# Kernel optimization log

Measured on AMD Instinct MI355X. Metric: run time of the kernel, lower is better.

The kernel has to match this reference:

```python
import jax, jax.numpy as jnp
import numpy as np

HEAD_DIM = 128
HIDDEN = 5120
NUM_KV_GROUPS = 8
NUM_MODALITIES = 3
NUM_Q_HEADS = 40
QKV_PER_MOD = NUM_Q_HEADS * HEAD_DIM + 2 * NUM_KV_GROUPS * HEAD_DIM + NUM_Q_HEADS  # 7208


def _rms_norm(x, w, eps=1e-6):
    xf = x.astype(jnp.float32)
    inv = jax.lax.rsqrt(jnp.mean(xf * xf, axis=-1, keepdims=True) + eps)
    return (xf * inv).astype(x.dtype) * w


def _apply_rope(x, cos, sin):
    # x: [B,S,H,D], cos/sin: [B,S,rd]
    rd = cos.shape[-1]
    xr, xp = x[..., :rd], x[..., rd:]
    c, s = cos[:, :, None, :], sin[:, :, None, :]
    x1, x2 = xr[..., : rd // 2], xr[..., rd // 2:]
    rot = jnp.concatenate([-x2, x1], axis=-1)
    return jnp.concatenate([xr * c + rot * s, xp], axis=-1)


def setup_inputs() -> dict:
    key = jax.random.key(0)
    ks = jax.random.split(key, 6)
    B, S = 1, 2048
    return {
        "x": jax.random.normal(ks[0], (B, S, HIDDEN), jnp.float32),
        "rope_cos": jax.random.uniform(ks[1], (B, S, HEAD_DIM), jnp.float32),
        "rope_sin": jax.random.uniform(ks[2], (B, S, HEAD_DIM), jnp.float32),
        "modality_ids": jax.random.randint(ks[3], (B, S), 0, NUM_MODALITIES, jnp.int32),
        "pre_norm": jnp.ones((NUM_MODALITIES * HIDDEN,), jnp.float32),
        "qkv_w": jax.random.normal(ks[4], (NUM_MODALITIES * QKV_PER_MOD, HIDDEN), jnp.float32) * 0.02,
        "q_norm": jnp.ones((NUM_MODALITIES * HEAD_DIM,), jnp.float32),
        "k_norm": jnp.ones((NUM_MODALITIES * HEAD_DIM,), jnp.float32),
        "proj_w": jax.random.normal(ks[5], (NUM_MODALITIES * HIDDEN, HIDDEN), jnp.float32) * 0.02,
    }


def reference(x, rope_cos, rope_sin, modality_ids, pre_norm, qkv_w, q_norm, k_norm, proj_w):
    B, S, _ = x.shape
    # per-token modality gather of pre-norm weight
    norm_w = pre_norm.reshape(NUM_MODALITIES, HIDDEN)[modality_ids]  # [B,S,H]
    normed = _rms_norm(x, norm_w)

    # modality-routed QKV: compute all modalities, select with one-hot (dense, jit-friendly)
    oh = jax.nn.one_hot(modality_ids, NUM_MODALITIES, dtype=x.dtype)  # [B,S,M]
    qkv_w3 = qkv_w.reshape(NUM_MODALITIES, QKV_PER_MOD, HIDDEN)
    qkv_all = jnp.einsum("bsh,moh->bsmo", normed, qkv_w3)  # [B,S,M,QKV]
    qkv = jnp.einsum("bsm,bsmo->bso", oh, qkv_all)

    q_dim = NUM_Q_HEADS * HEAD_DIM
    k_dim = NUM_KV_GROUPS * HEAD_DIM
    q = qkv[..., :q_dim].reshape(B, S, NUM_Q_HEADS, HEAD_DIM)
    k = qkv[..., q_dim:q_dim + k_dim].reshape(B, S, NUM_KV_GROUPS, HEAD_DIM)
    v = qkv[..., q_dim + k_dim:q_dim + 2 * k_dim].reshape(B, S, NUM_KV_GROUPS, HEAD_DIM)
    gate = jax.nn.sigmoid(qkv[..., q_dim + 2 * k_dim:q_dim + 2 * k_dim + NUM_Q_HEADS])  # [B,S,NQ]

    qn = q_norm.reshape(NUM_MODALITIES, HEAD_DIM)[modality_ids][:, :, None, :]  # [B,S,1,D]
    kn = k_norm.reshape(NUM_MODALITIES, HEAD_DIM)[modality_ids][:, :, None, :]
    q = _rms_norm(q, qn)
    k = _rms_norm(k, kn)

    q = _apply_rope(q, rope_cos, rope_sin)
    k = _apply_rope(k, rope_cos, rope_sin)

    repeat = NUM_Q_HEADS // NUM_KV_GROUPS
    k = jnp.repeat(k, repeat, axis=2)  # [B,S,NQ,D]
    v = jnp.repeat(v, repeat, axis=2)

    scale = 1.0 / np.sqrt(HEAD_DIM)
    scores = jnp.einsum("bqhd,bkhd->bhqk", q, k) * scale  # [B,NQ,S,S]
    attn = jax.nn.softmax(scores, axis=-1)
    out = jnp.einsum("bhqk,bkhd->bqhd", attn, v)  # [B,S,NQ,D]

    out = (out * gate[..., None]).reshape(B, S, NUM_Q_HEADS * HEAD_DIM)

    proj_w3 = proj_w.reshape(NUM_MODALITIES, HIDDEN, HIDDEN)
    proj_all = jnp.einsum("bsh,moh->bsmo", out, proj_w3)  # [B,S,M,H]
    return jnp.einsum("bsm,bsmo->bso", oh, proj_all)
```

## Files before the change

### kernel.cpp

```cpp
#include <hip/hip_runtime.h>

typedef _Float16 f16;
typedef f16 f16x8 __attribute__((ext_vector_type(8)));
typedef f16 f16x4 __attribute__((ext_vector_type(4)));
typedef float f32x4 __attribute__((ext_vector_type(4)));

#define HID 5120
#define QKVO 7208
#define S_TOK 2048
#define NQH 40
#define NKV 8
#define HD 128

__device__ __forceinline__ void gload16(const void* g, void* l) {
    __builtin_amdgcn_global_load_lds(
        (const __attribute__((address_space(1))) void*)g,
        (__attribute__((address_space(3))) void*)l,
        16, 0, 0);
}

__global__ void sort_tokens(const int* __restrict__ mod, int* __restrict__ sorted,
                            int* __restrict__ offs)
{
    int tid = threadIdx.x, wave = tid >> 6, lane = tid & 63;
    int mloc[8];
    int c[3] = {0, 0, 0};
#pragma unroll
    for (int j = 0; j < 8; ++j) {
        int m = mod[tid * 8 + j];
        mloc[j] = m;
        c[m]++;
    }
    __shared__ int wsum[4][3];
    int excl[3];
#pragma unroll
    for (int m = 0; m < 3; ++m) {
        int v = c[m];
        int incl = v;
        for (int d = 1; d < 64; d <<= 1) {
            int n = __shfl_up(incl, d, 64);
            if (lane >= d) incl += n;
        }
        excl[m] = incl - v;
        if (lane == 63) wsum[wave][m] = incl;
    }
    __syncthreads();
    int wbase[3], tot[3];
#pragma unroll
    for (int m = 0; m < 3; ++m) {
        int b = 0, t = 0;
        for (int w = 0; w < 4; ++w) {
            if (w < wave) b += wsum[w][m];
            t += wsum[w][m];
        }
        wbase[m] = b;
        tot[m] = t;
    }
    int base[3];
    base[0] = 0;
    base[1] = tot[0];
    base[2] = tot[0] + tot[1];
    if (tid == 0) {
        offs[0] = 0;
        offs[1] = tot[0];
        offs[2] = tot[0] + tot[1];
        offs[3] = S_TOK;
    }
    int pos[3];
#pragma unroll
    for (int m = 0; m < 3; ++m) pos[m] = base[m] + wbase[m] + excl[m];
#pragma unroll
    for (int j = 0; j < 8; ++j) {
        int m = mloc[j];
        sorted[pos[m]++] = tid * 8 + j;
    }
}

__global__ void cvt_f32_f16(const float* __restrict__ src, f16* __restrict__ dst, int n4)
{
    int i = blockIdx.x * 256 + threadIdx.x;
    int stride = gridDim.x * 256;
    const float4* s4 = (const float4*)src;
    f16x4* d4 = (f16x4*)dst;
    for (; i < n4; i += stride) {
        float4 a = s4[i];
        f16x4 h;
        h[0] = (f16)a.x; h[1] = (f16)a.y; h[2] = (f16)a.z; h[3] = (f16)a.w;
        d4[i] = h;
    }
}

__global__ void rms_pre(const float* __restrict__ x, const int* __restrict__ mod,
                        const float* __restrict__ prenorm, f16* __restrict__ A1)
{
    int tok = blockIdx.x, tid = threadIdx.x;
    int m = mod[tok];
    const float4* xv = (const float4*)(x + (size_t)tok * HID);
    float4 v[5];
    float ss = 0.f;
#pragma unroll
    for (int j = 0; j < 5; ++j) {
        v[j] = xv[tid + 256 * j];
        ss += v[j].x * v[j].x + v[j].y * v[j].y + v[j].z * v[j].z + v[j].w * v[j].w;
    }
    for (int d = 1; d < 64; d <<= 1) ss += __shfl_xor(ss, d, 64);
    __shared__ float ws[4];
    if ((tid & 63) == 0) ws[tid >> 6] = ss;
    __syncthreads();
    float tot = ws[0] + ws[1] + ws[2] + ws[3];
    float inv = rsqrtf(tot * (1.f / HID) + 1e-6f);
    const float4* wv = (const float4*)(prenorm + (size_t)m * HID);
    f16x4* out4 = (f16x4*)(A1 + (size_t)tok * HID);
#pragma unroll
    for (int j = 0; j < 5; ++j) {
        float4 w = wv[tid + 256 * j];
        f16x4 h;
        h[0] = (f16)(v[j].x * inv * w.x);
        h[1] = (f16)(v[j].y * inv * w.y);
        h[2] = (f16)(v[j].z * inv * w.z);
        h[3] = (f16)(v[j].w * inv * w.w);
        out4[tid + 256 * j] = h;
    }
}

__global__ void gemm_grouped(const f16* __restrict__ A, const f16* __restrict__ W,
                             float* __restrict__ C,
                             const int* __restrict__ sorted_tok,
                             const int* __restrict__ mod_off, int NW, int NTN, int NPAN)
{
    const int K = HID;
    int F = blockIdx.x;
    int g = F & 7, s = F >> 3;
    int P = (s >> 4) * 8 + g;
    if (P >= NPAN) return;
    int mt = s & 15;
    int nt = P % NTN, mod = P / NTN;
    int off = mod_off[mod], cnt = mod_off[mod + 1] - off;
    if (mt * 128 >= cnt) return;
    __shared__ __align__(16) f16 As[128 * 64];
    __shared__ __align__(16) f16 Bs[128 * 64];
    __shared__ int rowtok[128];
    int tid = threadIdx.x, wave = tid >> 6, lane = tid & 63;
    if (tid < 128) {
        int r = mt * 128 + tid;
        rowtok[tid] = (r < cnt) ? sorted_tok[off + r] : -1;
    }
    __syncthreads();
    int wr = wave >> 1, wc = wave & 1;
    f32x4 acc[4][4] = {};
    const f16* Wm = W + (size_t)mod * NW * K;
    for (int kt = 0; kt < K / 64; ++kt) {
        int k0 = kt * 64;
#pragma unroll
        for (int it = 0; it < 4; ++it) {
            int c = it * 256 + tid;
            int row = c >> 3, kc = c & 7, skc = kc ^ (row & 7);
            int tk = rowtok[row];
            if (tk < 0) tk = 0;
            gload16(A + (size_t)tk * K + k0 + skc * 8, &As[c * 8]);
        }
#pragma unroll
        for (int it = 0; it < 4; ++it) {
            int c = it * 256 + tid;
            int row = c >> 3, kc = c & 7, skc = kc ^ (row & 7);
            int o = nt * 128 + row;
            if (o >= NW) o = NW - 1;
            gload16(Wm + (size_t)o * K + k0 + skc * 8, &Bs[c * 8]);
        }
        __syncthreads();
#pragma unroll
        for (int ks = 0; ks < 2; ++ks) {
            f16x8 a[4], b[4];
#pragma unroll
            for (int i = 0; i < 4; ++i) {
                int ar = wr * 64 + i * 16 + (lane & 15);
                int ac = (ks * 4 + (lane >> 4)) ^ (ar & 7);
                a[i] = *(const f16x8*)&As[ar * 64 + ac * 8];
                int br = wc * 64 + i * 16 + (lane & 15);
                int bc = (ks * 4 + (lane >> 4)) ^ (br & 7);
                b[i] = *(const f16x8*)&Bs[br * 64 + bc * 8];
            }
#pragma unroll
            for (int mi = 0; mi < 4; ++mi)
#pragma unroll
                for (int nj = 0; nj < 4; ++nj)
                    acc[mi][nj] = __builtin_amdgcn_mfma_f32_16x16x32_f16(
                        a[mi], b[nj], acc[mi][nj], 0, 0, 0);
        }
        __syncthreads();
    }
    int cl = lane & 15, rg = lane >> 4;
#pragma unroll
    for (int mi = 0; mi < 4; ++mi) {
#pragma unroll
        for (int rr = 0; rr < 4; ++rr) {
            int row = wr * 64 + mi * 16 + rg * 4 + rr;
            int tk = rowtok[row];
            if (tk < 0) continue;
            float* crow = C + (size_t)tk * NW;
#pragma unroll
            for (int nj = 0; nj < 4; ++nj) {
                int o = nt * 128 + wc * 64 + nj * 16 + cl;
                if (o < NW) crow[o] = acc[mi][nj][rr];
            }
        }
    }
}

__global__ void qkv_post(const float* __restrict__ qkv, const int* __restrict__ mod,
                         const float* __restrict__ cosb, const float* __restrict__ sinb,
                         const float* __restrict__ qnorm, const float* __restrict__ knorm,
                         f16* __restrict__ Qb, f16* __restrict__ Kb, float* __restrict__ gateb)
{
    int tok = blockIdx.x, tid = threadIdx.x;
    int wave = tid >> 6, lane = tid & 63;
    int m = mod[tok];
    float c0 = cosb[tok * HD + lane], c1 = cosb[tok * HD + 64 + lane];
    float s0 = sinb[tok * HD + lane], s1 = sinb[tok * HD + 64 + lane];
    const float* row = qkv + (size_t)tok * QKVO;
    for (int u = wave; u < 48; u += 4) {
        int base = (u < 40) ? u * HD : NQH * HD + (u - 40) * HD;
        float x0 = row[base + lane];
        float x1 = row[base + 64 + lane];
        float ss = x0 * x0 + x1 * x1;
        for (int d = 1; d < 64; d <<= 1) ss += __shfl_xor(ss, d, 64);
        float inv = rsqrtf(ss * (1.f / HD) + 1e-6f);
        const float* nw = (u < 40 ? qnorm : knorm) + m * HD;
        float n0 = x0 * inv * nw[lane];
        float n1 = x1 * inv * nw[64 + lane];
        float r0 = n0 * c0 - n1 * s0;
        float r1 = n1 * c1 + n0 * s1;
        if (u < 40) {
            const float sc = 0.08838834764831845f;
            r0 *= sc; r1 *= sc;
            Qb[((size_t)u * S_TOK + tok) * HD + lane] = (f16)r0;
            Qb[((size_t)u * S_TOK + tok) * HD + 64 + lane] = (f16)r1;
        } else {
            Kb[((size_t)(u - 40) * S_TOK + tok) * HD + lane] = (f16)r0;
            Kb[((size_t)(u - 40) * S_TOK + tok) * HD + 64 + lane] = (f16)r1;
        }
    }
    if (tid < 40) {
        float g = row[NQH * HD + 2 * NKV * HD + tid];
        gateb[tok * 40 + tid] = 1.f / (1.f + __expf(-g));
    }
}

__global__ void vtrans(const float* __restrict__ qkv, f16* __restrict__ Vt)
{
    int tc = blockIdx.x;
    int g = blockIdx.y;
    int tid = threadIdx.x;
    __shared__ float tile[64][129];
#pragma unroll
    for (int it = 0; it < 8; ++it) {
        int idx = it * 256 + tid;
        int r = idx >> 5, c4 = idx & 31;
        float4 v = *(const float4*)(qkv + (size_t)(tc * 64 + r) * QKVO + NQH * HD + NKV * HD + g * HD + c4 * 4);
        tile[r][c4 * 4 + 0] = v.x;
        tile[r][c4 * 4 + 1] = v.y;
        tile[r][c4 * 4 + 2] = v.z;
        tile[r][c4 * 4 + 3] = v.w;
    }
    __syncthreads();
    int d = tid >> 1, half = tid & 1;
    f16* dst = Vt + ((size_t)g * HD + d) * S_TOK + tc * 64;
#pragma unroll
    for (int j = 0; j < 32; ++j) {
        int c = half * 32 + j;
        dst[c] = (f16)tile[16 * (c & 3) + (c >> 2)][d];
    }
}

__global__ __launch_bounds__(512, 4) void attn(
    const f16* __restrict__ Qb, const f16* __restrict__ Kb,
    const f16* __restrict__ Vtb, const float* __restrict__ gateb,
    f16* __restrict__ A2)
{
    int qt = blockIdx.x, h = blockIdx.y, grp = h / 5;
    int tid = threadIdx.x, wave = tid >> 6, lane = tid & 63;
    __shared__ __align__(16) char smem[81920];
    f16* Qs  = (f16*)smem;
    f16* Kb1 = (f16*)smem;
    char* pbase = smem + 16384 + wave * 2048;
    f16* Kb0 = (f16*)(smem + 32768);
    f16* Vb0 = (f16*)(smem + 49152);
    f16* Vb1 = (f16*)(smem + 65536);

    const f16* Qg = Qb + ((size_t)h * S_TOK + qt * 128) * HD;
    const f16* Kg = Kb + (size_t)grp * S_TOK * HD;
    const f16* Vg = Vtb + (size_t)grp * HD * S_TOK;

#pragma unroll
    for (int it = 0; it < 4; ++it) {
        int c = it * 512 + tid, row = c >> 4, kc = c & 15, skc = kc ^ (row & 15);
        gload16(Qg + row * HD + skc * 8, &Qs[c * 8]);
    }
#pragma unroll
    for (int it = 0; it < 2; ++it) {
        int c = it * 512 + tid, row = c >> 4, kc = c & 15, skc = kc ^ (row & 15);
        gload16(Kg + (size_t)row * HD + skc * 8, &Kb0[c * 8]);
    }
#pragma unroll
    for (int it = 0; it < 2; ++it) {
        int c = it * 512 + tid, row = c >> 3, kc = c & 7, skc = kc ^ (row & 7);
        gload16(Vg + (size_t)row * S_TOK + skc * 8, &Vb0[c * 8]);
    }
    asm volatile("s_waitcnt vmcnt(4)" ::: "memory");
    __builtin_amdgcn_s_barrier();
    f16x8 qf[4];
    {
        int row = wave * 16 + (lane & 15);
#pragma unroll
        for (int ks = 0; ks < 4; ++ks) {
            int sk = (ks * 4 + (lane >> 4)) ^ (row & 15);
            qf[ks] = *(const f16x8*)&Qs[row * 128 + sk * 8];
        }
    }
    asm volatile("s_waitcnt lgkmcnt(0)" ::: "memory");
    __builtin_amdgcn_s_barrier();

    f32x4 o[8] = {};
    float mrow[4] = {-3.0e38f, -3.0e38f, -3.0e38f, -3.0e38f};
    float lrow[4] = {0.f, 0.f, 0.f, 0.f};

    int cur = 0;
    for (int t = 0; t < 32; ++t) {
        f16* Ks = cur ? Kb1 : Kb0;
        f16* Vs = cur ? Vb1 : Vb0;
        if (t < 31) {
            f16* Kn = cur ? Kb0 : Kb1;
            f16* Vn = cur ? Vb0 : Vb1;
#pragma unroll
            for (int it = 0; it < 2; ++it) {
                int c = it * 512 + tid, row = c >> 4, kc = c & 15, skc = kc ^ (row & 15);
                gload16(Kg + (size_t)((t + 1) * 64 + row) * HD + skc * 8, &Kn[c * 8]);
            }
#pragma unroll
            for (int it = 0; it < 2; ++it) {
                int c = it * 512 + tid, row = c >> 3, kc = c & 7, skc = kc ^ (row & 7);
                gload16(Vg + (size_t)row * S_TOK + (t + 1) * 64 + skc * 8, &Vn[c * 8]);
            }
            asm volatile("s_waitcnt vmcnt(4)" ::: "memory");
        } else {
            asm volatile("s_waitcnt vmcnt(0)" ::: "memory");
        }
        __builtin_amdgcn_s_barrier();

        f32x4 s[4] = {};
        __builtin_amdgcn_s_setprio(1);
#pragma unroll
        for (int ks = 0; ks < 4; ++ks) {
#pragma unroll
            for (int nj = 0; nj < 4; ++nj) {
                int kr = nj * 16 + (lane & 15);
                int sk = (ks * 4 + (lane >> 4)) ^ (kr & 15);
                f16x8 kf = *(const f16x8*)&Ks[kr * 128 + sk * 8];
                s[nj] = __builtin_amdgcn_mfma_f32_16x16x32_f16(qf[ks], kf, s[nj], 0, 0, 0);
            }
        }
        __builtin_amdgcn_s_setprio(0);
        float mx[4], psum[4];
#pragma unroll
        for (int r = 0; r < 4; ++r)
            mx[r] = fmaxf(fmaxf(s[0][r], s[1][r]), fmaxf(s[2][r], s[3][r]));
        for (int d = 1; d < 16; d <<= 1) {
#pragma unroll
            for (int r = 0; r < 4; ++r) mx[r] = fmaxf(mx[r], __shfl_xor(mx[r], d, 16));
        }
        bool need = false;
#pragma unroll
        for (int r = 0; r < 4; ++r) need = need || (mx[r] > mrow[r] + 8.f);
        if (__any(need)) {
#pragma unroll
            for (int r = 0; r < 4; ++r) {
                float nm = fmaxf(mrow[r], mx[r]);
                float corr = __expf(mrow[r] - nm);
                mrow[r] = nm;
                lrow[r] *= corr;
#pragma unroll
                for (int nj2 = 0; nj2 < 8; ++nj2) o[nj2][r] *= corr;
            }
        }
#pragma unroll
        for (int r = 0; r < 4; ++r) psum[r] = 0.f;
#pragma unroll
        for (int r = 0; r < 4; ++r) {
            f16x4 hp;
#pragma unroll
            for (int nj = 0; nj < 4; ++nj) {
                float p = __expf(s[nj][r] - mrow[r]);
                psum[r] += p;
                hp[nj] = (f16)p;
            }
            int q = (lane >> 4) * 4 + r;
            int addr = q * 128 + ((8 * (lane & 15)) ^ ((q & 7) << 4));
            *(f16x4*)(pbase + addr) = hp;
        }
        for (int d = 1; d < 16; d <<= 1) {
#pragma unroll
            for (int r = 0; r < 4; ++r) psum[r] += __shfl_xor(psum[r], d, 16);
        }
#pragma unroll
        for (int r = 0; r < 4; ++r) lrow[r] += psum[r];
        __builtin_amdgcn_s_setprio(1);
#pragma unroll
        for (int ks2 = 0; ks2 < 2; ++ks2) {
            int prow = lane & 15;
            int sk = (ks2 * 4 + (lane >> 4)) ^ (prow & 7);
            f16x8 pa = *(const f16x8*)(pbase + prow * 128 + sk * 16);
#pragma unroll
            for (int nj2 = 0; nj2 < 8; ++nj2) {
                int vr = nj2 * 16 + (lane & 15);
                int skv = (ks2 * 4 + (lane >> 4)) ^ (vr & 7);
                f16x8 vf = *(const f16x8*)&Vs[vr * 64 + skv * 8];
                o[nj2] = __builtin_amdgcn_mfma_f32_16x16x32_f16(pa, vf, o[nj2], 0, 0, 0);
            }
        }
        __builtin_amdgcn_s_setprio(0);
        asm volatile("s_waitcnt lgkmcnt(0)" ::: "memory");
        __builtin_amdgcn_s_barrier();
        cur ^= 1;
    }
    int rbase = qt * 128 + wave * 16 + (lane >> 4) * 4;
#pragma unroll
    for (int r = 0; r < 4; ++r) {
        int tok = rbase + r;
        float sc = gateb[tok * 40 + h] / lrow[r];
#pragma unroll
        for (int nj2 = 0; nj2 < 8; ++nj2) {
            int d = nj2 * 16 + (lane & 15);
            A2[(size_t)tok * HID + h * HD + d] = (f16)(o[nj2][r] * sc);
        }
    }
}

extern "C" void kernel_launch(void* const* d_in, const int* in_sizes, int n_in,
                              void* d_out, int out_size, void* d_ws, size_t ws_size,
                              hipStream_t stream)
{
    const float* x = (const float*)d_in[0];
    const float* rc = (const float*)d_in[1];
    const float* rs = (const float*)d_in[2];
    const int* mod = (const int*)d_in[3];
    const float* prenorm = (const float*)d_in[4];
    const float* qkvw = (const float*)d_in[5];
    const float* qn = (const float*)d_in[6];
    const float* kn = (const float*)d_in[7];
    const float* projw = (const float*)d_in[8];
    float* out = (float*)d_out;

    char* p = (char*)d_ws;
    auto alloc = [&](size_t bytes) {
        char* r = p;
        p += (bytes + 255) & ~(size_t)255;
        return r;
    };
    int* sorted = (int*)alloc(S_TOK * 4);
    int* offs = (int*)alloc(16);
    f16* A1 = (f16*)alloc((size_t)S_TOK * HID * 2);
    f16* Wq = (f16*)alloc((size_t)3 * QKVO * HID * 2);
    f16* Wp = (f16*)alloc((size_t)3 * HID * HID * 2);
    float* qkv = (float*)alloc((size_t)S_TOK * QKVO * 4);
    f16* Qb = (f16*)alloc((size_t)NQH * S_TOK * HD * 2);
    f16* Kb = (f16*)alloc((size_t)NKV * S_TOK * HD * 2);
    f16* Vt = (f16*)alloc((size_t)NKV * HD * S_TOK * 2);
    float* gate = (float*)alloc((size_t)S_TOK * 40 * 4);
    f16* A2 = (f16*)alloc((size_t)S_TOK * HID * 2);
    if ((size_t)(p - (char*)d_ws) > ws_size) return;

    sort_tokens<<<1, 256, 0, stream>>>(mod, sorted, offs);
    cvt_f32_f16<<<2048, 256, 0, stream>>>(qkvw, Wq, 3 * QKVO * HID / 4);
    cvt_f32_f16<<<2048, 256, 0, stream>>>(projw, Wp, 3 * HID * HID / 4);
    rms_pre<<<2048, 256, 0, stream>>>(x, mod, prenorm, A1);
    {
        int NTN = 57, NPAN = NTN * 3;
        int grid = 8 * ((NPAN + 7) / 8) * 16;
        gemm_grouped<<<grid, 256, 0, stream>>>(A1, Wq, qkv, sorted, offs, QKVO, NTN, NPAN);
    }
    qkv_post<<<2048, 256, 0, stream>>>(qkv, mod, rc, rs, qn, kn, Qb, Kb, gate);
    vtrans<<<dim3(32, 8), 256, 0, stream>>>(qkv, Vt);
    attn<<<dim3(16, 40), 512, 0, stream>>>(Qb, Kb, Vt, gate, A2);
    {
        int NTN = 40, NPAN = NTN * 3;
        int grid = 8 * ((NPAN + 7) / 8) * 16;
        gemm_grouped<<<grid, 256, 0, stream>>>(A2, Wp, out, sorted, offs, HID, NTN, NPAN);
    }
}
```

Baseline: 834.1 us.

## Double-buffer LDS tiles in grouped GEMM to overlap global loads with MFMA

The grouped GEMM now keeps two LDS buffers for each of the A and B tiles. It issues the async global-to-LDS loads for the next K tile before computing on the current one, and uses a partial vmcnt wait so only the current tile's loads must finish. This is meant to hide global memory latency behind the MFMA work instead of stalling on every K step. In exchange it doubles LDS use (about 64KB per block), which may reduce occupancy, and it depends on hand-written waitcnt values being correct.

```diff
diff --git a/kernel.cpp b/kernel.cpp
--- a/kernel.cpp
+++ b/kernel.cpp
@@ -129,6 +129,7 @@
                              const int* __restrict__ mod_off, int NW, int NTN, int NPAN)
 {
     const int K = HID;
+    const int NKT = K / 64;
     int F = blockIdx.x;
     int g = F & 7, s = F >> 3;
     int P = (s >> 4) * 8 + g;
@@ -137,8 +138,8 @@
     int nt = P % NTN, mod = P / NTN;
     int off = mod_off[mod], cnt = mod_off[mod + 1] - off;
     if (mt * 128 >= cnt) return;
-    __shared__ __align__(16) f16 As[128 * 64];
-    __shared__ __align__(16) f16 Bs[128 * 64];
+    __shared__ __align__(16) f16 As[2][128 * 64];
+    __shared__ __align__(16) f16 Bs[2][128 * 64];
     __shared__ int rowtok[128];
     int tid = threadIdx.x, wave = tid >> 6, lane = tid & 63;
     if (tid < 128) {
@@ -146,28 +147,52 @@
         rowtok[tid] = (r < cnt) ? sorted_tok[off + r] : -1;
     }
     __syncthreads();
+    const f16* Wm = W + (size_t)mod * NW * K;
     int wr = wave >> 1, wc = wave & 1;
     f32x4 acc[4][4] = {};
-    const f16* Wm = W + (size_t)mod * NW * K;
-    for (int kt = 0; kt < K / 64; ++kt) {
-        int k0 = kt * 64;
-#pragma unroll
-        for (int it = 0; it < 4; ++it) {
-            int c = it * 256 + tid;
-            int row = c >> 3, kc = c & 7, skc = kc ^ (row & 7);
-            int tk = rowtok[row];
-            if (tk < 0) tk = 0;
-            gload16(A + (size_t)tk * K + k0 + skc * 8, &As[c * 8]);
-        }
-#pragma unroll
-        for (int it = 0; it < 4; ++it) {
-            int c = it * 256 + tid;
-            int row = c >> 3, kc = c & 7, skc = kc ^ (row & 7);
-            int o = nt * 128 + row;
-            if (o >= NW) o = NW - 1;
-            gload16(Wm + (size_t)o * K + k0 + skc * 8, &Bs[c * 8]);
-        }
-        __syncthreads();
+
+#pragma unroll
+    for (int it = 0; it < 4; ++it) {
+        int c = it * 256 + tid;
+        int row = c >> 3, kc = c & 7, skc = kc ^ (row & 7);
+        int tk = rowtok[row];
+        if (tk < 0) tk = 0;
+        gload16(A + (size_t)tk * K + skc * 8, &As[0][c * 8]);
+    }
+#pragma unroll
+    for (int it = 0; it < 4; ++it) {
+        int c = it * 256 + tid;
+        int row = c >> 3, kc = c & 7, skc = kc ^ (row & 7);
+        int o = nt * 128 + row;
+        if (o >= NW) o = NW - 1;
+        gload16(Wm + (size_t)o * K + skc * 8, &Bs[0][c * 8]);
+    }
+
+    int cur = 0;
+    for (int kt = 0; kt < NKT; ++kt) {
+        if (kt < NKT - 1) {
+            int k1 = (kt + 1) * 64;
+#pragma unroll
+            for (int it = 0; it < 4; ++it) {
+                int c = it * 256 + tid;
+                int row = c >> 3, kc = c & 7, skc = kc ^ (row & 7);
+                int tk = rowtok[row];
+                if (tk < 0) tk = 0;
+                gload16(A + (size_t)tk * K + k1 + skc * 8, &As[cur ^ 1][c * 8]);
+            }
+#pragma unroll
+            for (int it = 0; it < 4; ++it) {
+                int c = it * 256 + tid;
+                int row = c >> 3, kc = c & 7, skc = kc ^ (row & 7);
+                int o = nt * 128 + row;
+                if (o >= NW) o = NW - 1;
+                gload16(Wm + (size_t)o * K + k1 + skc * 8, &Bs[cur ^ 1][c * 8]);
+            }
+            asm volatile("s_waitcnt vmcnt(8)" ::: "memory");
+        } else {
+            asm volatile("s_waitcnt vmcnt(0)" ::: "memory");
+        }
+        __builtin_amdgcn_s_barrier();
 #pragma unroll
         for (int ks = 0; ks < 2; ++ks) {
             f16x8 a[4], b[4];
@@ -175,10 +200,10 @@
             for (int i = 0; i < 4; ++i) {
                 int ar = wr * 64 + i * 16 + (lane & 15);
                 int ac = (ks * 4 + (lane >> 4)) ^ (ar & 7);
-                a[i] = *(const f16x8*)&As[ar * 64 + ac * 8];
+                a[i] = *(const f16x8*)&As[cur][ar * 64 + ac * 8];
                 int br = wc * 64 + i * 16 + (lane & 15);
                 int bc = (ks * 4 + (lane >> 4)) ^ (br & 7);
-                b[i] = *(const f16x8*)&Bs[br * 64 + bc * 8];
+                b[i] = *(const f16x8*)&Bs[cur][br * 64 + bc * 8];
             }
 #pragma unroll
             for (int mi = 0; mi < 4; ++mi)
@@ -187,7 +212,9 @@
                     acc[mi][nj] = __builtin_amdgcn_mfma_f32_16x16x32_f16(
                         a[mi], b[nj], acc[mi][nj], 0, 0, 0);
         }
-        __syncthreads();
+        asm volatile("s_waitcnt lgkmcnt(0)" ::: "memory");
+        __builtin_amdgcn_s_barrier();
+        cur ^= 1;
     }
     int cl = lane & 15, rg = lane >> 4;
 #pragma unroll
```

Result: slower. 960.3 us (+15.1%).

## Replace grouped GEMM with 256x256 double-buffered 8-wave pipelined kernel

Applied to the files above, without the earlier changes.

Rewrites the modality-grouped GEMM to use 256x256 output tiles with 512 threads (8 waves), double-buffered LDS staging, and an interleaved schedule where async global->LDS loads for the next k-tile are issued between MFMA quarters, with s_setprio raised around MFMA bursts. The aim is more data reuse per tile and overlap of memory latency with compute, replacing the single-buffered load-sync-compute loop. It raises LDS use to about 128KB per block and register pressure (acc[8][4]), which may reduce occupancy. Larger tiles also waste more work on partially filled M tiles per modality and on the padded N edge of the QKV output (7208 columns).

```diff
diff --git a/kernel.cpp b/kernel.cpp
--- a/kernel.cpp
+++ b/kernel.cpp
@@ -123,85 +123,182 @@
     }
 }
 
-__global__ void gemm_grouped(const f16* __restrict__ A, const f16* __restrict__ W,
-                             float* __restrict__ C,
-                             const int* __restrict__ sorted_tok,
-                             const int* __restrict__ mod_off, int NW, int NTN, int NPAN)
+__global__ __launch_bounds__(512, 2) void gemm_grouped8(
+    const f16* __restrict__ A, const f16* __restrict__ W,
+    float* __restrict__ C,
+    const int* __restrict__ sorted_tok,
+    const int* __restrict__ mod_off, int NW, int NTN, int NPAN)
 {
     const int K = HID;
+    const int NIT = K / 128;
     int F = blockIdx.x;
     int g = F & 7, s = F >> 3;
-    int P = (s >> 4) * 8 + g;
+    int P = (s >> 3) * 8 + g;
     if (P >= NPAN) return;
-    int mt = s & 15;
+    int mt = s & 7;
     int nt = P % NTN, mod = P / NTN;
     int off = mod_off[mod], cnt = mod_off[mod + 1] - off;
-    if (mt * 128 >= cnt) return;
-    __shared__ __align__(16) f16 As[128 * 64];
-    __shared__ __align__(16) f16 Bs[128 * 64];
-    __shared__ int rowtok[128];
+    if (mt * 256 >= cnt) return;
+
+    __shared__ __align__(16) f16 As[2][256 * 64];
+    __shared__ __align__(16) f16 Bs[2][256 * 64];
+    __shared__ int rowtok[256];
     int tid = threadIdx.x, wave = tid >> 6, lane = tid & 63;
-    if (tid < 128) {
-        int r = mt * 128 + tid;
+    if (tid < 256) {
+        int r = mt * 256 + tid;
         rowtok[tid] = (r < cnt) ? sorted_tok[off + r] : -1;
     }
     __syncthreads();
-    int wr = wave >> 1, wc = wave & 1;
-    f32x4 acc[4][4] = {};
     const f16* Wm = W + (size_t)mod * NW * K;
-    for (int kt = 0; kt < K / 64; ++kt) {
-        int k0 = kt * 64;
-#pragma unroll
-        for (int it = 0; it < 4; ++it) {
-            int c = it * 256 + tid;
-            int row = c >> 3, kc = c & 7, skc = kc ^ (row & 7);
+
+    int aoff[2][2], boff[2][2];
+#pragma unroll
+    for (int h = 0; h < 2; ++h) {
+#pragma unroll
+        for (int l = 0; l < 2; ++l) {
+            int c = l * 512 + tid;
+            int rl = c >> 3, kc = c & 7, skc = kc ^ (rl & 7);
+            int row = h * 128 + rl;
             int tk = rowtok[row];
             if (tk < 0) tk = 0;
-            gload16(A + (size_t)tk * K + k0 + skc * 8, &As[c * 8]);
-        }
-#pragma unroll
-        for (int it = 0; it < 4; ++it) {
-            int c = it * 256 + tid;
-            int row = c >> 3, kc = c & 7, skc = kc ^ (row & 7);
-            int o = nt * 128 + row;
+            aoff[h][l] = tk * K + skc * 8;
+            int o = nt * 256 + row;
             if (o >= NW) o = NW - 1;
-            gload16(Wm + (size_t)o * K + k0 + skc * 8, &Bs[c * 8]);
-        }
-        __syncthreads();
-#pragma unroll
-        for (int ks = 0; ks < 2; ++ks) {
-            f16x8 a[4], b[4];
-#pragma unroll
-            for (int i = 0; i < 4; ++i) {
-                int ar = wr * 64 + i * 16 + (lane & 15);
+            boff[h][l] = o * K + skc * 8;
+        }
+    }
+    int dsto = tid * 8;
+
+    int wr = wave >> 2, wc = wave & 3;
+    f32x4 acc[8][4] = {};
+
+    auto STAGE_A = [&](int b, int h, int kt) {
+#pragma unroll
+        for (int l = 0; l < 2; ++l)
+            gload16(A + aoff[h][l] + kt * 64, &As[b][h * 8192 + l * 4096 + dsto]);
+    };
+    auto STAGE_B = [&](int b, int h, int kt) {
+#pragma unroll
+        for (int l = 0; l < 2; ++l)
+            gload16(Wm + boff[h][l] + kt * 64, &Bs[b][h * 8192 + l * 4096 + dsto]);
+    };
+
+    f16x8 bf[2][4];
+    auto LOAD_B = [&](int b) {
+#pragma unroll
+        for (int ks = 0; ks < 2; ++ks)
+#pragma unroll
+            for (int j = 0; j < 4; ++j) {
+                int br = wc * 64 + j * 16 + (lane & 15);
+                int bc = (ks * 4 + (lane >> 4)) ^ (br & 7);
+                bf[ks][j] = *(const f16x8*)&Bs[b][br * 64 + bc * 8];
+            }
+    };
+    f16x8 af[2][2];
+    auto LOAD_A = [&](int b, int q) {
+#pragma unroll
+        for (int ks = 0; ks < 2; ++ks)
+#pragma unroll
+            for (int i = 0; i < 2; ++i) {
+                int ar = wr * 128 + (q * 2 + i) * 16 + (lane & 15);
                 int ac = (ks * 4 + (lane >> 4)) ^ (ar & 7);
-                a[i] = *(const f16x8*)&As[ar * 64 + ac * 8];
-                int br = wc * 64 + i * 16 + (lane & 15);
-                int bc = (ks * 4 + (lane >> 4)) ^ (br & 7);
-                b[i] = *(const f16x8*)&Bs[br * 64 + bc * 8];
-            }
-#pragma unroll
-            for (int mi = 0; mi < 4; ++mi)
-#pragma unroll
-                for (int nj = 0; nj < 4; ++nj)
-                    acc[mi][nj] = __builtin_amdgcn_mfma_f32_16x16x32_f16(
-                        a[mi], b[nj], acc[mi][nj], 0, 0, 0);
-        }
-        __syncthreads();
-    }
+                af[ks][i] = *(const f16x8*)&As[b][ar * 64 + ac * 8];
+            }
+    };
+    auto MFMA_Q = [&](int q) {
+        __builtin_amdgcn_s_setprio(1);
+#pragma unroll
+        for (int ks = 0; ks < 2; ++ks)
+#pragma unroll
+            for (int i = 0; i < 2; ++i)
+#pragma unroll
+                for (int j = 0; j < 4; ++j)
+                    acc[q * 2 + i][j] = __builtin_amdgcn_mfma_f32_16x16x32_f16(
+                        af[ks][i], bf[ks][j], acc[q * 2 + i][j], 0, 0, 0);
+        __builtin_amdgcn_s_setprio(0);
+    };
+
+    STAGE_A(0, 0, 0); STAGE_A(0, 1, 0); STAGE_B(0, 0, 0); STAGE_B(0, 1, 0);
+
+    for (int it = 0; it < NIT; ++it) {
+        int kt0 = 2 * it, kt1 = kt0 + 1;
+        STAGE_A(1, 0, kt1);
+        asm volatile("s_waitcnt vmcnt(2)" ::: "memory");
+        __builtin_amdgcn_s_barrier();
+        LOAD_B(0);
+        LOAD_A(0, 0);
+        MFMA_Q(0);
+        asm volatile("" ::: "memory");
+        __builtin_amdgcn_s_barrier();
+        LOAD_A(0, 1);
+        STAGE_A(1, 1, kt1);
+        asm volatile("" ::: "memory");
+        __builtin_amdgcn_s_barrier();
+        MFMA_Q(1);
+        asm volatile("" ::: "memory");
+        __builtin_amdgcn_s_barrier();
+        LOAD_A(0, 2);
+        STAGE_B(1, 0, kt1);
+        asm volatile("" ::: "memory");
+        __builtin_amdgcn_s_barrier();
+        MFMA_Q(2);
+        asm volatile("" ::: "memory");
+        __builtin_amdgcn_s_barrier();
+        LOAD_A(0, 3);
+        STAGE_B(1, 1, kt1);
+        asm volatile("" ::: "memory");
+        __builtin_amdgcn_s_barrier();
+        MFMA_Q(3);
+        asm volatile("" ::: "memory");
+        __builtin_amdgcn_s_barrier();
+        if (it < NIT - 1) {
+            STAGE_A(0, 0, kt0 + 2);
+            asm volatile("s_waitcnt vmcnt(2)" ::: "memory");
+        } else {
+            asm volatile("s_waitcnt vmcnt(0)" ::: "memory");
+        }
+        __builtin_amdgcn_s_barrier();
+        LOAD_B(1);
+        LOAD_A(1, 0);
+        MFMA_Q(0);
+        asm volatile("" ::: "memory");
+        __builtin_amdgcn_s_barrier();
+        LOAD_A(1, 1);
+        if (it < NIT - 1) STAGE_A(0, 1, kt0 + 2);
+        asm volatile("" ::: "memory");
+        __builtin_amdgcn_s_barrier();
+        MFMA_Q(1);
+        asm volatile("" ::: "memory");
+        __builtin_amdgcn_s_barrier();
+        LOAD_A(1, 2);
+        if (it < NIT - 1) STAGE_B(0, 0, kt0 + 2);
+        asm volatile("" ::: "memory");
+        __builtin_amdgcn_s_barrier();
+        MFMA_Q(2);
+        asm volatile("" ::: "memory");
+        __builtin_amdgcn_s_barrier();
+        LOAD_A(1, 3);
+        if (it < NIT - 1) STAGE_B(0, 1, kt0 + 2);
+        asm volatile("" ::: "memory");
+        __builtin_amdgcn_s_barrier();
+        MFMA_Q(3);
+        asm volatile("" ::: "memory");
+        __builtin_amdgcn_s_barrier();
+    }
+
     int cl = lane & 15, rg = lane >> 4;
 #pragma unroll
-    for (int mi = 0; mi < 4; ++mi) {
+    for (int fi = 0; fi < 8; ++fi) {
 #pragma unroll
         for (int rr = 0; rr < 4; ++rr) {
-            int row = wr * 64 + mi * 16 + rg * 4 + rr;
+            int row = wr * 128 + fi * 16 + rg * 4 + rr;
             int tk = rowtok[row];
             if (tk < 0) continue;
             float* crow = C + (size_t)tk * NW;
 #pragma unroll
-            for (int nj = 0; nj < 4; ++nj) {
-                int o = nt * 128 + wc * 64 + nj * 16 + cl;
-                if (o < NW) crow[o] = acc[mi][nj][rr];
+            for (int j = 0; j < 4; ++j) {
+                int o = nt * 256 + wc * 64 + j * 16 + cl;
+                if (o < NW) crow[o] = acc[fi][j][rr];
             }
         }
     }
@@ -474,16 +571,16 @@
     cvt_f32_f16<<<2048, 256, 0, stream>>>(projw, Wp, 3 * HID * HID / 4);
     rms_pre<<<2048, 256, 0, stream>>>(x, mod, prenorm, A1);
     {
-        int NTN = 57, NPAN = NTN * 3;
-        int grid = 8 * ((NPAN + 7) / 8) * 16;
-        gemm_grouped<<<grid, 256, 0, stream>>>(A1, Wq, qkv, sorted, offs, QKVO, NTN, NPAN);
+        int NTN = (QKVO + 255) / 256, NPAN = NTN * 3;
+        int grid = ((NPAN + 7) / 8) * 8 * 8;
+        gemm_grouped8<<<grid, 512, 0, stream>>>(A1, Wq, qkv, sorted, offs, QKVO, NTN, NPAN);
     }
     qkv_post<<<2048, 256, 0, stream>>>(qkv, mod, rc, rs, qn, kn, Qb, Kb, gate);
     vtrans<<<dim3(32, 8), 256, 0, stream>>>(qkv, Vt);
     attn<<<dim3(16, 40), 512, 0, stream>>>(Qb, Kb, Vt, gate, A2);
     {
-        int NTN = 40, NPAN = NTN * 3;
-        int grid = 8 * ((NPAN + 7) / 8) * 16;
-        gemm_grouped<<<grid, 256, 0, stream>>>(A2, Wp, out, sorted, offs, HID, NTN, NPAN);
-    }
-}
+        int NTN = HID / 256, NPAN = NTN * 3;
+        int grid = ((NPAN + 7) / 8) * 8 * 8;
+        gemm_grouped8<<<grid, 512, 0, stream>>>(A2, Wp, out, sorted, offs, HID, NTN, NPAN);
+    }
+}
```

New measurement: 942.8 us. 1.13x slower.
